# Kernel tuning notes

Measured on AMD Instinct MI355X. Metric: run time of the kernel, lower is better.

Reference implementation:

```python
import jax, jax.numpy as jnp
import numpy as np

B, D, S = 16, 512, 1500   # batch, input_size, seq_len
E, K, L = 8, 1024, 8      # embedding_size, num_embeddings, num_layers
TAU = 1.0
EPS = 1e-12               # F.normalize default eps


def setup_inputs() -> dict:
    key = jax.random.key(0)
    ks = jax.random.split(key, 5)
    x = jax.random.normal(ks[0], (B, D, S), dtype=jnp.float32)
    # weight-norm parametrized 1x1 conv params (v direction, g magnitude, bias)
    in_v = jax.random.normal(ks[1], (L, E, D), dtype=jnp.float32) * 0.05
    in_g = jnp.ones((L, E), dtype=jnp.float32)
    in_b = jnp.zeros((L, E), dtype=jnp.float32)
    out_v = jax.random.normal(ks[2], (L, D, E), dtype=jnp.float32) * 0.05
    out_g = jnp.ones((L, D), dtype=jnp.float32)
    out_b = jnp.zeros((L, D), dtype=jnp.float32)
    codebook = jax.random.normal(ks[3], (L, K, E), dtype=jnp.float32)
    return dict(x=x, in_v=in_v, in_g=in_g, in_b=in_b,
                out_v=out_v, out_g=out_g, out_b=out_b, codebook=codebook)


def _wn(v, g):
    # torch weight_norm (dim=0): w = g * v / ||v|| with norm over all dims except out-channel
    n = jnp.sqrt(jnp.sum(v * v, axis=1, keepdims=True))
    return g[:, None] * v / n


def _l2norm(x):
    # F.normalize(p=2, eps=1e-12)
    n = jnp.linalg.norm(x, axis=-1, keepdims=True)
    return x / jnp.maximum(n, EPS)


def _vq_layer(xr, iv, ig, ib, ov, og, ob, cb):
    Wi = _wn(iv, ig)                                              # [E, D]
    x_proj = jnp.einsum('ed,bds->bes', Wi, xr) + ib[:, None]      # [B, E, S]
    xf = x_proj.transpose(0, 2, 1).reshape(B * S, E)              # [B*S, E]
    xn = _l2norm(xf)
    cn = _l2norm(cb)                                              # [K, E]
    dist = (jnp.sum(xn * xn, axis=1, keepdims=True)
            - 2.0 * (xn @ cn.T)
            + jnp.sum(cn * cn, axis=1)[None, :])                  # [B*S, K]
    logits = -dist / TAU
    idxs = jnp.argmax(-dist, axis=1).reshape(B, S)                # [B, S]
    xq = cb[idxs].transpose(0, 2, 1)                              # [B, E, S] (un-normalized codebook)
    commit = jnp.mean((x_proj - jax.lax.stop_gradient(xq)) ** 2, axis=(1, 2))  # per-batch
    cbloss = jnp.mean((xq - jax.lax.stop_gradient(x_proj)) ** 2, axis=(1, 2))
    xq_st = x_proj + jax.lax.stop_gradient(xq - x_proj)           # straight-through
    Wo = _wn(ov, og)                                              # [D, E]
    xq_out = jnp.einsum('de,bes->bds', Wo, xq_st) + ob[:, None]   # [B, D, S]
    return xq_out, logits, idxs, commit, cbloss


def reference(x, in_v, in_g, in_b, out_v, out_g, out_b, codebook):
    # eval mode: all layers active, mask all-ones => masked mean == plain batch mean
    xq_sum = jnp.zeros_like(x)
    xr = x
    idxs_l, logits_l = [], []
    commit = jnp.float32(0.0)
    cbl = jnp.float32(0.0)
    for i in range(L):
        xq, lg, ix, cl, bl = _vq_layer(xr, in_v[i], in_g[i], in_b[i],
                                       out_v[i], out_g[i], out_b[i], codebook[i])
        xq_sum = xq_sum + xq
        xr = xr - xq
        commit = commit + jnp.mean(cl)
        cbl = cbl + jnp.mean(bl)
        idxs_l.append(ix)
        logits_l.append(lg)
    x_idxs = jnp.stack(idxs_l, axis=1)     # [B, L, S]
    x_logits = jnp.stack(logits_l, axis=1) # [B*S, L, K]
    return xq_sum, x_idxs, x_logits, commit, cbl
```

## Files before the change

### kernel.cpp

```cpp
#include <hip/hip_runtime.h>

constexpr int Lx = 8;
constexpr int Bx = 16;
constexpr int Dx = 512;
constexpr int Sx = 1500;
constexpr int Ex = 8;
constexpr int Kx = 1024;
constexpr int BS = Bx * Sx;
#define EPSF 1e-12f

__global__ __launch_bounds__(64) void k_wn_in(const float* __restrict__ v,
                                              const float* __restrict__ g,
                                              float* __restrict__ WiT) {
    int row = blockIdx.x;
    int l = row >> 3, e = row & 7;
    int lane = threadIdx.x;
    const float* vr = v + row * Dx;
    float s = 0.f;
    for (int j = lane; j < Dx; j += 64) { float t = vr[j]; s += t * t; }
    for (int off = 32; off; off >>= 1) s += __shfl_down(s, off);
    s = __shfl(s, 0);
    float scale = g[row] / sqrtf(s);
    for (int j = lane; j < Dx; j += 64)
        WiT[((size_t)l * Dx + j) * Ex + e] = vr[j] * scale;
}

__global__ __launch_bounds__(256) void k_wn_out_cb(const float* __restrict__ ov,
                                                   const float* __restrict__ og,
                                                   const float* __restrict__ cb,
                                                   float* __restrict__ Wo,
                                                   float* __restrict__ cn,
                                                   float* __restrict__ cc,
                                                   double* __restrict__ acc) {
    int r = blockIdx.x * blockDim.x + threadIdx.x;
    if (r == 0) *acc = 0.0;
    if (r < Lx * Dx) {
        const float* vr = ov + r * Ex;
        float s = 0.f;
        #pragma unroll
        for (int e = 0; e < Ex; e++) s += vr[e] * vr[e];
        float sc = og[r] / sqrtf(s);
        #pragma unroll
        for (int e = 0; e < Ex; e++) Wo[r * Ex + e] = vr[e] * sc;
    } else {
        int q = r - Lx * Dx;
        if (q < Lx * Kx) {
            const float* vr = cb + q * Ex;
            float s = 0.f;
            #pragma unroll
            for (int e = 0; e < Ex; e++) s += vr[e] * vr[e];
            float n = fmaxf(sqrtf(s), EPSF);
            float s2 = 0.f, qv[Ex];
            #pragma unroll
            for (int e = 0; e < Ex; e++) { qv[e] = vr[e] / n; s2 += qv[e] * qv[e]; }
            #pragma unroll
            for (int e = 0; e < Ex; e++) cn[q * Ex + e] = qv[e];
            cc[q] = s2;
        }
    }
}

__global__ __launch_bounds__(256, 3) void k_mega(const float* __restrict__ x,
                                                 const float* __restrict__ WiT,
                                                 const float* __restrict__ ibias,
                                                 const float* __restrict__ Wo,
                                                 const float* __restrict__ obias,
                                                 const float* __restrict__ cb,
                                                 const float* __restrict__ cn,
                                                 const float* __restrict__ cc,
                                                 float* __restrict__ out0,
                                                 float* __restrict__ oidx,
                                                 float* __restrict__ logits,
                                                 double* __restrict__ acc) {
    __shared__ float4 cnA[Kx];
    __shared__ float4 cnB[Kx];
    __shared__ float  ccs[Kx];
    __shared__ float  red[8 * Ex * 32];
    __shared__ float  xprojs[Ex * 32];
    __shared__ float  xqs[Ex * 32];
    __shared__ float  bred[4];

    const int t = threadIdx.x;
    const int col = t & 31;
    const int g = t >> 5;
    const int wave = t >> 6, lane = t & 63;
    const int c = blockIdx.x * 32 + col;
    const int b = c / Sx;
    const int s = c - b * Sx;
    const float* xcol = x + (size_t)b * Dx * Sx + s;

    float xr[64];
    #pragma unroll
    for (int i = 0; i < 64; i++) xr[i] = xcol[(size_t)(g * 64 + i) * Sx];

    float lossp = 0.f;

    for (int l = 0; l < Lx; l++) {
        const float4* cn4 = (const float4*)(cn + (size_t)l * Kx * Ex);
        for (int i2 = t; i2 < Kx; i2 += 256) {
            cnA[i2] = cn4[i2 * 2];
            cnB[i2] = cn4[i2 * 2 + 1];
            ccs[i2] = cc[l * Kx + i2];
        }
        __syncthreads();

        const float4* wt = (const float4*)(WiT + (size_t)l * Dx * Ex);
        float pacc[8] = {0, 0, 0, 0, 0, 0, 0, 0};
        #pragma unroll
        for (int i = 0; i < 64; i++) {
            int d = g * 64 + i;
            float4 w0 = wt[d * 2 + 0];
            float4 w1 = wt[d * 2 + 1];
            float v = xr[i];
            pacc[0] += w0.x * v; pacc[1] += w0.y * v;
            pacc[2] += w0.z * v; pacc[3] += w0.w * v;
            pacc[4] += w1.x * v; pacc[5] += w1.y * v;
            pacc[6] += w1.z * v; pacc[7] += w1.w * v;
        }
        #pragma unroll
        for (int e = 0; e < 8; e++) red[(g * 8 + e) * 32 + col] = pacc[e];
        __syncthreads();

        {
            float sum = 0.f;
            #pragma unroll
            for (int gg = 0; gg < 8; gg++) sum += red[(gg * 8 + g) * 32 + col];
            xprojs[g * 32 + col] = sum + ibias[l * Ex + g];
        }
        __syncthreads();

        for (int pass = 0; pass < 2; pass++) {
            const int colbase = wave * 8 + pass * 4;
            float xn[4][8];
            float xc[4], best[4];
            int bk[4];
            float* lrow[4];
            #pragma unroll
            for (int c4 = 0; c4 < 4; c4++) {
                int mycol = colbase + c4;
                int mc = blockIdx.x * 32 + mycol;
                float xp[8]; float xx2 = 0.f;
                #pragma unroll
                for (int e = 0; e < 8; e++) {
                    xp[e] = xprojs[e * 32 + mycol];
                    xx2 += xp[e] * xp[e];
                }
                float nrm = fmaxf(sqrtf(xx2), EPSF);
                float xx = 0.f;
                #pragma unroll
                for (int e = 0; e < 8; e++) {
                    xn[c4][e] = xp[e] / nrm;
                    xx += xn[c4][e] * xn[c4][e];
                }
                xc[c4] = xx;
                best[c4] = -3.0e38f;
                bk[c4] = 0;
                lrow[c4] = logits + ((size_t)mc * Lx + l) * Kx;
            }
            #pragma unroll 2
            for (int j = 0; j < 16; j++) {
                int k = j * 64 + lane;
                float4 a  = cnA[k];
                float4 b4 = cnB[k];
                float  cv = ccs[k];
                #pragma unroll
                for (int c4 = 0; c4 < 4; c4++) {
                    float dot = xn[c4][0] * a.x  + xn[c4][1] * a.y +
                                xn[c4][2] * a.z  + xn[c4][3] * a.w +
                                xn[c4][4] * b4.x + xn[c4][5] * b4.y +
                                xn[c4][6] * b4.z + xn[c4][7] * b4.w;
                    float lg = -(xc[c4] - 2.f * dot + cv);
                    lrow[c4][k] = lg;
                    if (lg > best[c4]) { best[c4] = lg; bk[c4] = k; }
                }
            }
            #pragma unroll
            for (int c4 = 0; c4 < 4; c4++) {
                float bv = best[c4]; int bi = bk[c4];
                for (int off = 32; off; off >>= 1) {
                    float ov = __shfl_xor(bv, off);
                    int   oi = __shfl_xor(bi, off);
                    if (ov > bv || (ov == bv && oi < bi)) { bv = ov; bi = oi; }
                }
                int mycol = colbase + c4;
                int mc = blockIdx.x * 32 + mycol;
                int mb = mc / Sx, ms = mc - mb * Sx;
                if (lane == 0) oidx[((size_t)mb * Lx + l) * Sx + ms] = (float)bi;
                if (lane < 8) {
                    float q = cb[((size_t)l * Kx + bi) * Ex + lane];
                    xqs[lane * 32 + mycol] = q;
                    float dl = xprojs[lane * 32 + mycol] - q;
                    lossp += dl * dl;
                }
            }
        }
        __syncthreads();

        float xq[8];
        #pragma unroll
        for (int e = 0; e < 8; e++) xq[e] = xqs[e * 32 + col];
        const float4* wo4 = (const float4*)(Wo + (size_t)l * Dx * Ex);
        const float* obl = obias + l * Dx;
        #pragma unroll
        for (int i = 0; i < 64; i++) {
            int d = g * 64 + i;
            float4 w0 = wo4[d * 2 + 0];
            float4 w1 = wo4[d * 2 + 1];
            float dsum = w0.x * xq[0] + w0.y * xq[1] + w0.z * xq[2] + w0.w * xq[3] +
                         w1.x * xq[4] + w1.y * xq[5] + w1.z * xq[6] + w1.w * xq[7] +
                         obl[d];
            xr[i] -= dsum;
        }
    }

    float* ocol = out0 + (size_t)b * Dx * Sx + s;
    #pragma unroll
    for (int i = 0; i < 64; i++) {
        float xv = xcol[(size_t)(g * 64 + i) * Sx];
        ocol[(size_t)(g * 64 + i) * Sx] = xv - xr[i];
    }

    for (int off = 32; off; off >>= 1) lossp += __shfl_down(lossp, off);
    if (lane == 0) bred[wave] = lossp;
    __syncthreads();
    if (t == 0)
        atomicAdd(acc, (double)(bred[0] + bred[1] + bred[2] + bred[3]));
}

__global__ void k_scalar(const double* __restrict__ acc,
                         float* __restrict__ commit, float* __restrict__ cbl) {
    if (threadIdx.x == 0) {
        float v = (float)(*acc / (double)((size_t)Bx * Ex * Sx));
        *commit = v;
        *cbl = v;
    }
}

extern "C" void kernel_launch(void* const* d_in, const int* in_sizes, int n_in,
                              void* d_out, int out_size, void* d_ws, size_t ws_size,
                              hipStream_t stream) {
    const float* x     = (const float*)d_in[0];
    const float* in_v  = (const float*)d_in[1];
    const float* in_g  = (const float*)d_in[2];
    const float* in_b  = (const float*)d_in[3];
    const float* out_v = (const float*)d_in[4];
    const float* out_g = (const float*)d_in[5];
    const float* out_b = (const float*)d_in[6];
    const float* cb    = (const float*)d_in[7];

    float* out = (float*)d_out;
    float* out0     = out;
    float* oidx     = out + 12288000;
    float* ologits  = out + 12480000;
    float* ocommit  = out + 209088000;
    float* ocbl     = out + 209088001;

    char* w = (char*)d_ws;
    float*  WiT   = (float*)(w);
    float*  Wo    = (float*)(w + 131072);
    float*  cn    = (float*)(w + 262144);
    float*  cc    = (float*)(w + 524288);
    double* acc   = (double*)(w + 557056);

    k_wn_in<<<Lx * Ex, 64, 0, stream>>>(in_v, in_g, WiT);
    k_wn_out_cb<<<(Lx * Dx + Lx * Kx) / 256, 256, 0, stream>>>(out_v, out_g, cb,
                                                               Wo, cn, cc, acc);
    k_mega<<<BS / 32, 256, 0, stream>>>(x, WiT, in_b, Wo, out_b, cb, cn, cc,
                                        out0, oidx, ologits, acc);
    k_scalar<<<1, 64, 0, stream>>>(acc, ocommit, ocbl);
}
```

Measured before the change: 637.9 us.

## Transpose codebook in LDS and write logits as nontemporal float4 stores

The normalized codebook is now stored in shared memory transposed by embedding dimension, so each lane handles four consecutive codes at once and computes their dot products with packed vector FMAs. Logits are written as 16-byte nontemporal vector stores instead of scalar stores, aiming to cut store instruction count and cache pollution for the large logits tensor. The argmax tie order is kept because each lane still scans its codes in ascending order. The transposed LDS fill uses strided scalar writes, which may cause bank conflicts, and the extra accumulators raise register pressure.

```diff
diff --git a/kernel.cpp b/kernel.cpp
--- a/kernel.cpp
+++ b/kernel.cpp
@@ -8,6 +8,8 @@
 constexpr int Kx = 1024;
 constexpr int BS = Bx * Sx;
 #define EPSF 1e-12f
+
+typedef __attribute__((ext_vector_type(4))) float f32x4;
 
 __global__ __launch_bounds__(64) void k_wn_in(const float* __restrict__ v,
                                               const float* __restrict__ g,
@@ -72,13 +74,12 @@
                                                  float* __restrict__ oidx,
                                                  float* __restrict__ logits,
                                                  double* __restrict__ acc) {
-    __shared__ float4 cnA[Kx];
-    __shared__ float4 cnB[Kx];
-    __shared__ float  ccs[Kx];
-    __shared__ float  red[8 * Ex * 32];
-    __shared__ float  xprojs[Ex * 32];
-    __shared__ float  xqs[Ex * 32];
-    __shared__ float  bred[4];
+    __shared__ f32x4 cne4[Ex][Kx / 4];
+    __shared__ f32x4 ccs4[Kx / 4];
+    __shared__ float red[8 * Ex * 32];
+    __shared__ float xprojs[Ex * 32];
+    __shared__ float xqs[Ex * 32];
+    __shared__ float bred[4];
 
     const int t = threadIdx.x;
     const int col = t & 31;
@@ -98,9 +99,17 @@
     for (int l = 0; l < Lx; l++) {
         const float4* cn4 = (const float4*)(cn + (size_t)l * Kx * Ex);
         for (int i2 = t; i2 < Kx; i2 += 256) {
-            cnA[i2] = cn4[i2 * 2];
-            cnB[i2] = cn4[i2 * 2 + 1];
-            ccs[i2] = cc[l * Kx + i2];
+            float4 w0 = cn4[i2 * 2];
+            float4 w1 = cn4[i2 * 2 + 1];
+            ((float*)cne4[0])[i2] = w0.x;
+            ((float*)cne4[1])[i2] = w0.y;
+            ((float*)cne4[2])[i2] = w0.z;
+            ((float*)cne4[3])[i2] = w0.w;
+            ((float*)cne4[4])[i2] = w1.x;
+            ((float*)cne4[5])[i2] = w1.y;
+            ((float*)cne4[6])[i2] = w1.z;
+            ((float*)cne4[7])[i2] = w1.w;
+            ((float*)ccs4)[i2] = cc[l * Kx + i2];
         }
         __syncthreads();
 
@@ -157,21 +166,34 @@
                 bk[c4] = 0;
                 lrow[c4] = logits + ((size_t)mc * Lx + l) * Kx;
             }
-            #pragma unroll 2
-            for (int j = 0; j < 16; j++) {
-                int k = j * 64 + lane;
-                float4 a  = cnA[k];
-                float4 b4 = cnB[k];
-                float  cv = ccs[k];
+            for (int j = 0; j < 4; j++) {
+                const int v4 = j * 64 + lane;
+                const int k0 = v4 * 4;
+                f32x4 acc0 = {0.f, 0.f, 0.f, 0.f};
+                f32x4 acc1 = {0.f, 0.f, 0.f, 0.f};
+                f32x4 acc2 = {0.f, 0.f, 0.f, 0.f};
+                f32x4 acc3 = {0.f, 0.f, 0.f, 0.f};
+                #pragma unroll
+                for (int e = 0; e < 8; e++) {
+                    f32x4 ce = cne4[e][v4];
+                    acc0 += xn[0][e] * ce;
+                    acc1 += xn[1][e] * ce;
+                    acc2 += xn[2][e] * ce;
+                    acc3 += xn[3][e] * ce;
+                }
+                f32x4 cv = ccs4[v4];
                 #pragma unroll
                 for (int c4 = 0; c4 < 4; c4++) {
-                    float dot = xn[c4][0] * a.x  + xn[c4][1] * a.y +
-                                xn[c4][2] * a.z  + xn[c4][3] * a.w +
-                                xn[c4][4] * b4.x + xn[c4][5] * b4.y +
-                                xn[c4][6] * b4.z + xn[c4][7] * b4.w;
-                    float lg = -(xc[c4] - 2.f * dot + cv);
-                    lrow[c4][k] = lg;
-                    if (lg > best[c4]) { best[c4] = lg; bk[c4] = k; }
+                    f32x4 dv = (c4 == 0) ? acc0 : (c4 == 1) ? acc1
+                             : (c4 == 2) ? acc2 : acc3;
+                    f32x4 lg;
+                    #pragma unroll
+                    for (int u = 0; u < 4; u++) {
+                        float l_ = -(xc[c4] - 2.f * dv[u] + cv[u]);
+                        lg[u] = l_;
+                        if (l_ > best[c4]) { best[c4] = l_; bk[c4] = k0 + u; }
+                    }
+                    __builtin_nontemporal_store(lg, (f32x4*)(lrow[c4] + k0));
                 }
             }
             #pragma unroll
```

Result: slower. 805.2 us (+26.2%).

## Defer logits writes to a separate kernel, stashing normalized inputs in output rows

Applied to the files above, without the earlier changes.

The mega kernel no longer writes the 1024 logits per row per layer while computing argmax. Instead it stores the normalized projection and its squared norm in the first slots of each logits row. A new kernel reads those values back, recomputes the dot products against the normalized codebook held in shared memory, and overwrites each row in full. This aims to take the large logits store stream off the sequential layer loop's critical path. It costs an extra kernel and a recompute of the distances, and the mega kernel's argmax and the logits kernel must agree numerically.

```diff
diff --git a/kernel.cpp b/kernel.cpp
--- a/kernel.cpp
+++ b/kernel.cpp
@@ -134,7 +134,6 @@
             float xn[4][8];
             float xc[4], best[4];
             int bk[4];
-            float* lrow[4];
             #pragma unroll
             for (int c4 = 0; c4 < 4; c4++) {
                 int mycol = colbase + c4;
@@ -155,7 +154,15 @@
                 xc[c4] = xx;
                 best[c4] = -3.0e38f;
                 bk[c4] = 0;
-                lrow[c4] = logits + ((size_t)mc * Lx + l) * Kx;
+                if (lane == 0) {
+                    float* rh = logits + ((size_t)mc * Lx + l) * Kx;
+                    float4 v0 = {xn[c4][0], xn[c4][1], xn[c4][2], xn[c4][3]};
+                    float4 v1 = {xn[c4][4], xn[c4][5], xn[c4][6], xn[c4][7]};
+                    float4 v2 = {xx, 0.f, 0.f, 0.f};
+                    *(float4*)(rh)     = v0;
+                    *(float4*)(rh + 4) = v1;
+                    *(float4*)(rh + 8) = v2;
+                }
             }
             #pragma unroll 2
             for (int j = 0; j < 16; j++) {
@@ -170,7 +177,6 @@
                                 xn[c4][4] * b4.x + xn[c4][5] * b4.y +
                                 xn[c4][6] * b4.z + xn[c4][7] * b4.w;
                     float lg = -(xc[c4] - 2.f * dot + cv);
-                    lrow[c4][k] = lg;
                     if (lg > best[c4]) { best[c4] = lg; bk[c4] = k; }
                 }
             }
@@ -225,6 +231,44 @@
     __syncthreads();
     if (t == 0)
         atomicAdd(acc, (double)(bred[0] + bred[1] + bred[2] + bred[3]));
+}
+
+__global__ __launch_bounds__(256, 4) void k_logits(const float* __restrict__ cn,
+                                                   const float* __restrict__ cc,
+                                                   float* __restrict__ logits) {
+    __shared__ float4 cnA[Kx];
+    __shared__ float4 cnB[Kx];
+    __shared__ float  ccs[Kx];
+    const int t = threadIdx.x;
+    const int wave = t >> 6, lane = t & 63;
+    const int l = blockIdx.x / 100;
+    const int chunk = blockIdx.x - l * 100;
+
+    const float4* cn4 = (const float4*)(cn + (size_t)l * Kx * Ex);
+    for (int i = t; i < Kx; i += 256) {
+        cnA[i] = cn4[i * 2];
+        cnB[i] = cn4[i * 2 + 1];
+        ccs[i] = cc[l * Kx + i];
+    }
+    __syncthreads();
+
+    const int cbase = chunk * 240 + wave * 60;
+    for (int ci = 0; ci < 60; ci++) {
+        int c = cbase + ci;
+        float* lrow = logits + ((size_t)c * Lx + l) * Kx;
+        float4 x0 = *(const float4*)(lrow);
+        float4 x1 = *(const float4*)(lrow + 4);
+        float  xx = lrow[8];
+        #pragma unroll 4
+        for (int j = 0; j < 16; j++) {
+            int k = j * 64 + lane;
+            float4 a  = cnA[k];
+            float4 b4 = cnB[k];
+            float dot = x0.x * a.x  + x0.y * a.y + x0.z * a.z  + x0.w * a.w +
+                        x1.x * b4.x + x1.y * b4.y + x1.z * b4.z + x1.w * b4.w;
+            lrow[k] = -(xx - 2.f * dot + ccs[k]);
+        }
+    }
 }
 
 __global__ void k_scalar(const double* __restrict__ acc,
@@ -267,5 +311,6 @@
                                                                Wo, cn, cc, acc);
     k_mega<<<BS / 32, 256, 0, stream>>>(x, WiT, in_b, Wo, out_b, cb, cn, cc,
                                         out0, oidx, ologits, acc);
+    k_logits<<<Lx * 100, 256, 0, stream>>>(cn, cc, ologits);
     k_scalar<<<1, 64, 0, stream>>>(acc, ocommit, ocbl);
 }
```

New measurement: 784.5 us. 1.23x slower.
